# Performance work log

Measured on AMD Instinct MI355X. Metric: run time of the kernel, lower is better.

The kernel has to match this reference:

```python
import jax, jax.numpy as jnp
import numpy as np

EPS = 1e-7  # keras.backend.epsilon()
ROUTING_ITERS = 3

def squash(v, axis=-1):
    s2 = jnp.sum(jnp.square(v), axis=axis, keepdims=True)
    scale = s2 / (1.0 + s2) / jnp.sqrt(s2 + EPS)
    return scale * v

def setup_inputs() -> dict:
    key = jax.random.key(0)
    k1, k2 = jax.random.split(key)
    B, N_IN, D_IN = 128, 648, 16
    N_OUT, D_OUT = 32, 32
    x = jax.random.normal(k1, (B, N_IN, D_IN), dtype=jnp.float32)
    # glorot-uniform-ish scale for W: shape (N_in, num_caps, cap_dim, d_in)
    limit = np.sqrt(6.0 / (D_IN + D_OUT)).astype(np.float32)
    W = jax.random.uniform(k2, (N_IN, N_OUT, D_OUT, D_IN), dtype=jnp.float32,
                           minval=-limit, maxval=limit)
    return {"x": x, "W": W}

def reference(x, W):
    # prediction vectors u_hat: [B, N_in, N_out, D_out]
    # (original tiles inputs then matmuls W @ u; einsum fuses this)
    u_hat = jnp.einsum('njdi,bni->bnjd', W, x)
    B, N_in, N_out, _ = u_hat.shape
    logits = jnp.zeros((B, N_in, N_out, 1), dtype=u_hat.dtype)
    v = None
    for i in range(ROUTING_ITERS):
        c = jax.nn.softmax(logits, axis=2)                      # [B,N_in,N_out,1]
        s = jnp.sum(c * u_hat, axis=1, keepdims=True)           # [B,1,N_out,D_out]
        v = squash(s, axis=-1)                                  # [B,1,N_out,D_out]
        if i < ROUTING_ITERS - 1:
            agreement = jnp.sum(u_hat * v, axis=-1, keepdims=True)
            logits = logits + agreement
    return jnp.squeeze(v, axis=1)                               # [B,N_out,D_out]
```

## Files before the change

### kernel.cpp

```cpp
#include <hip/hip_runtime.h>
#include <hip/hip_fp16.h>
#include <math.h>


#define N_IN 648
#define ELEMS 131072

#define XF_OFF 65536
#define VLD 69632
#define LG 135168
#define ARENA_PH 139264
#define ARENA_P0 132608

typedef __attribute__((ext_vector_type(8))) _Float16 f16x8;
typedef __attribute__((ext_vector_type(16))) float f32x16;

union F16U { uint4 u; f16x8 f; };
union HU { __half h; unsigned short us; };

__device__ __forceinline__ unsigned pkh(float a, float b) {
  HU x, y; x.h = __float2half(a); y.h = __float2half(b);
  return (unsigned)x.us | ((unsigned)y.us << 16);
}
__device__ __forceinline__ float h2f(unsigned short u) {
  HU x; x.us = u; return __half2float(x.h);
}

__device__ __forceinline__ void writeW(char* wbuf, int jS, int d, const float4* r) {
  uint4 h0, h1;
  h0.x = pkh(r[0].x, r[0].y); h0.y = pkh(r[0].z, r[0].w);
  h0.z = pkh(r[1].x, r[1].y); h0.w = pkh(r[1].z, r[1].w);
  h1.x = pkh(r[2].x, r[2].y); h1.y = pkh(r[2].z, r[2].w);
  h1.z = pkh(r[3].x, r[3].y); h1.w = pkh(r[3].z, r[3].w);
  *(uint4*)(wbuf + jS * 1024 + d * 16) = h0;
  *(uint4*)(wbuf + jS * 1024 + 512 + d * 16) = h1;
}
__device__ __forceinline__ void loadW(float4* r, const float* __restrict__ W,
                                      int n, int jS, int d) {
  const float4* rp = (const float4*)(W + (size_t)n * 16384 + jS * 512 + d * 16);
  r[0] = rp[0]; r[1] = rp[1]; r[2] = rp[2]; r[3] = rp[3];
}

__device__ __forceinline__ void store_parts(char* arena, float* __restrict__ parts,
                                            const f32x16* acc, float scale,
                                            int nchunk, int b0, int t) {
  const int w = t >> 6, l = t & 63;
  const int b32 = l & 31, half = l >> 5;
  __syncthreads();
#pragma unroll
  for (int q = 0; q < 4; ++q) {
    const int j = w * 4 + q;
#pragma unroll
    for (int g = 0; g < 4; ++g) {
      float4 v4;
      v4.x = acc[q][g * 4 + 0] * scale;
      v4.y = acc[q][g * 4 + 1] * scale;
      v4.z = acc[q][g * 4 + 2] * scale;
      v4.w = acc[q][g * 4 + 3] * scale;
      *(float4*)(arena + (b32 * 1036 + j * 32 + g * 8 + 4 * half) * 4) = v4;
    }
  }
  __syncthreads();
  float* pb = parts + (size_t)nchunk * ELEMS + (size_t)b0 * 1024;
  const int rb = t >> 4, c16 = t & 15;
#pragma unroll
  for (int q = 0; q < 16; ++q) {
    const int e4 = c16 + q * 16;
    const float4 v4 = *(const float4*)(arena + (rb * 1036 + e4 * 4) * 4);
    *(float4*)(pb + rb * 1024 + e4 * 4) = v4;
  }
}

__device__ __forceinline__ void decode_bid(int bid, int NC, int& nchunk, int& btile) {
  if ((NC & 7) == 0) {
    const int r = bid & 7;
    btile = (bid >> 3) & 3;
    nchunk = (bid >> 5) * 8 + r;
  } else {
    nchunk = bid >> 2;
    btile = bid & 3;
  }
}

__global__ __launch_bounds__(512, 1) void caps_pass0_mfma(
    const float* __restrict__ x, const float* __restrict__ W,
    float* __restrict__ parts, int NC)
{
  __shared__ __align__(16) char arena[ARENA_P0];
  const int t = threadIdx.x;
  const int w = t >> 6, l = t & 63;
  const int jS = t >> 4, m = t & 15;
  int nchunk, btile;
  decode_bid(blockIdx.x, NC, nchunk, btile);
  const int n0 = (N_IN * nchunk) / NC;
  const int n1 = (N_IN * (nchunk + 1)) / NC;
  const int b0 = btile * 32;

  f32x16 acc[4];
#pragma unroll
  for (int q = 0; q < 4; ++q) acc[q] = (f32x16)(0.0f);

  {
    float4 rA[4], rB[4];
    loadW(rA, W, n0, jS, m);
    loadW(rB, W, n0, jS, m + 16);
    writeW(arena, jS, m, rA);
    writeW(arena, jS, m + 16, rB);
    if (t < 64) {
      const float4* xp = (const float4*)(x + ((size_t)(b0 + (t & 31)) * N_IN + n0) * 16 + (t >> 5) * 8);
      *(float4*)(arena + XF_OFF + t * 16) = xp[0];
      *(float4*)(arena + XF_OFF + 1024 + t * 16) = xp[1];
    }
  }

  int cur = 0;
  for (int n = n0; n < n1; ++n) {
    __syncthreads();
    const char* wf = arena + cur * 32768;
    const char* xb = arena + XF_OFF + cur * 2048;
    char* nwf = arena + (cur ^ 1) * 32768;
    char* nxb = arena + XF_OFF + (cur ^ 1) * 2048;
    const bool more = (n + 1 < n1);

    float4 tA[4], tB[4], xt0, xt1;
    if (more) {
      loadW(tA, W, n + 1, jS, m);
      loadW(tB, W, n + 1, jS, m + 16);
      if (t < 64) {
        const float4* xp = (const float4*)(x + ((size_t)(b0 + (t & 31)) * N_IN + n + 1) * 16 + (t >> 5) * 8);
        xt0 = xp[0]; xt1 = xp[1];
      }
    }

    const float4 xw0 = *(const float4*)(xb + l * 16);
    const float4 xw1 = *(const float4*)(xb + 1024 + l * 16);
    F16U bf;
    bf.u = uint4{pkh(xw0.x, xw0.y), pkh(xw0.z, xw0.w),
                 pkh(xw1.x, xw1.y), pkh(xw1.z, xw1.w)};
#pragma unroll
    for (int q = 0; q < 4; ++q) {
      const int j = w * 4 + q;
      const f16x8 af = *(const f16x8*)(wf + j * 1024 + l * 16);
      acc[q] = __builtin_amdgcn_mfma_f32_32x32x16_f16(af, bf.f, acc[q], 0, 0, 0);
    }

    if (more) {
      writeW(nwf, jS, m, tA);
      writeW(nwf, jS, m + 16, tB);
      if (t < 64) {
        *(float4*)(nxb + t * 16) = xt0;
        *(float4*)(nxb + 1024 + t * 16) = xt1;
      }
    }
    cur ^= 1;
  }
  store_parts(arena, parts, acc, 0.03125f, nchunk, b0, t);
}

__global__ __launch_bounds__(512, 1) void caps_phase_mfma(
    const float* __restrict__ x, const float* __restrict__ W,
    const float* __restrict__ v,
    float* __restrict__ parts, int NC)
{
  __shared__ __align__(16) char arena[ARENA_PH];
  const int t = threadIdx.x;
  const int w = t >> 6, l = t & 63;
  const int b32 = l & 31;
  const int jS = t >> 4, m = t & 15;
  int nchunk, btile;
  decode_bid(blockIdx.x, NC, nchunk, btile);
  const int n0 = (N_IN * nchunk) / NC;
  const int n1 = (N_IN * (nchunk + 1)) / NC;
  const int b0 = btile * 32;

#pragma unroll
  for (int r2 = 0; r2 < 2; ++r2) {
    const int j = t >> 4, b = (t & 15) + r2 * 16;
    const float4* gv = (const float4*)(v + (size_t)(b0 + b) * 1024 + j * 32);
    float4 g[8];
#pragma unroll
    for (int q = 0; q < 8; ++q) g[q] = gv[q];
#pragma unroll
    for (int h = 0; h < 2; ++h)
#pragma unroll
      for (int wd = 0; wd < 2; ++wd) {
        const float4 a = g[4 * wd + h];
        const float4 bb = g[4 * wd + h + 2];
        *(uint4*)(arena + VLD + j * 2048 + wd * 1024 + (h * 32 + b) * 16) =
            uint4{pkh(a.x, a.y), pkh(a.z, a.w), pkh(bb.x, bb.y), pkh(bb.z, bb.w)};
      }
  }

  {
    float4 rA[4], rB[4];
    loadW(rA, W, n0, jS, m);
    loadW(rB, W, n0, jS, m + 16);
    writeW(arena, jS, m, rA);
    writeW(arena, jS, m + 16, rB);
    if (t < 64) {
      const float4* xp = (const float4*)(x + ((size_t)(b0 + (t & 31)) * N_IN + n0) * 16 + (t >> 5) * 8);
      *(float4*)(arena + XF_OFF + t * 16) = xp[0];
      *(float4*)(arena + XF_OFF + 1024 + t * 16) = xp[1];
    }
  }

  f32x16 acc[4];
#pragma unroll
  for (int q = 0; q < 4; ++q) acc[q] = (f32x16)(0.0f);

  int cur = 0;
  for (int n = n0; n < n1; ++n) {
    __syncthreads();
    const char* wf = arena + cur * 32768;
    const char* xb = arena + XF_OFF + cur * 2048;
    char* nwf = arena + (cur ^ 1) * 32768;
    char* nxb = arena + XF_OFF + (cur ^ 1) * 2048;
    const bool more = (n + 1 < n1);

    float4 tA[4], xt0, xt1;
    if (more) {
      loadW(tA, W, n + 1, jS, m);
      if (t < 64) {
        const float4* xp = (const float4*)(x + ((size_t)(b0 + (t & 31)) * N_IN + n + 1) * 16 + (t >> 5) * 8);
        xt0 = xp[0]; xt1 = xp[1];
      }
    }

    const float4 xw0 = *(const float4*)(xb + l * 16);
    const float4 xw1 = *(const float4*)(xb + 1024 + l * 16);
    F16U bf;
    bf.u = uint4{pkh(xw0.x, xw0.y), pkh(xw0.z, xw0.w),
                 pkh(xw1.x, xw1.y), pkh(xw1.z, xw1.w)};

#pragma unroll
    for (int q = 0; q < 4; ++q) {
      const int j = w * 4 + q;
      const f16x8 af = *(const f16x8*)(wf + j * 1024 + l * 16);
      f32x16 ut = (f32x16)(0.0f);
      ut = __builtin_amdgcn_mfma_f32_32x32x16_f16(af, bf.f, ut, 0, 0, 0);
      const uint4 va = *(const uint4*)(arena + VLD + j * 2048 + l * 16);
      const uint4 vb = *(const uint4*)(arena + VLD + j * 2048 + 1024 + l * 16);
      const unsigned wd[8] = {va.x, va.y, va.z, va.w, vb.x, vb.y, vb.z, vb.w};
      float a = 0.f;
#pragma unroll
      for (int k = 0; k < 16; ++k) {
        const unsigned short us = (k & 1) ? (unsigned short)(wd[k >> 1] >> 16)
                                          : (unsigned short)(wd[k >> 1] & 0xFFFF);
        a = fmaf(ut[k], h2f(us), a);
      }
      a += __shfl_xor(a, 32);
      if (l < 32)
        *(float*)(arena + LG + (j * 32 + ((b32 ^ j) & 31)) * 4) = a;
    }
    __syncthreads();

    {
      const int jj = t & 31;
#pragma unroll
      for (int r = 0; r < 2; ++r) {
        const int b = r * 16 + (t >> 5);
        float* slot = (float*)(arena + LG + (jj * 32 + ((b ^ jj) & 31)) * 4);
        float lgv = *slot;
        float mx = lgv;
#pragma unroll
        for (int off = 16; off >= 1; off >>= 1) mx = fmaxf(mx, __shfl_xor(mx, off));
        const float e = __expf(lgv - mx);
        float Z = e;
#pragma unroll
        for (int off = 16; off >= 1; off >>= 1) Z += __shfl_xor(Z, off);
        *slot = e / Z;
      }
    }
    if (more) {
      writeW(nwf, jS, m, tA);
      loadW(tA, W, n + 1, jS, m + 16);
      if (t < 64) {
        *(float4*)(nxb + t * 16) = xt0;
        *(float4*)(nxb + 1024 + t * 16) = xt1;
      }
    }
    __syncthreads();

#pragma unroll
    for (int q = 0; q < 4; ++q) {
      const int j = w * 4 + q;
      const float cj = *(const float*)(arena + LG + (j * 32 + ((b32 ^ j) & 31)) * 4);
      F16U yf;
      yf.u = uint4{pkh(cj * xw0.x, cj * xw0.y), pkh(cj * xw0.z, cj * xw0.w),
                   pkh(cj * xw1.x, cj * xw1.y), pkh(cj * xw1.z, cj * xw1.w)};
      const f16x8 af = *(const f16x8*)(wf + j * 1024 + l * 16);
      acc[q] = __builtin_amdgcn_mfma_f32_32x32x16_f16(af, yf.f, acc[q], 0, 0, 0);
    }
    if (more) writeW(nwf, jS, m + 16, tA);
    cur ^= 1;
  }
  store_parts(arena, parts, acc, 1.0f, nchunk, b0, t);
}

__global__ void reduce_squash(const float* __restrict__ parts, int NC,
                              float* __restrict__ out,
                              const float* __restrict__ addprev) {
  const int e = blockIdx.x * 256 + threadIdx.x;
  float s = 0.f;
  for (int c = 0; c < NC; ++c) s += parts[(size_t)c * ELEMS + e];
  float s2 = s * s;
#pragma unroll
  for (int off = 16; off >= 1; off >>= 1) s2 += __shfl_xor(s2, off);
  const float scale = (s2 / (1.0f + s2)) * rsqrtf(s2 + 1e-7f);
  const float val = s * scale;
  out[e] = addprev ? (addprev[e] + val) : val;
}

extern "C" void kernel_launch(void* const* d_in, const int* in_sizes, int n_in,
                              void* d_out, int out_size, void* d_ws, size_t ws_size,
                              hipStream_t stream) {
  const float* x = (const float*)d_in[0];
  const float* W = (const float*)d_in[1];
  float* out = (float*)d_out;

  float* v0 = (float*)d_ws;
  float* vsum = v0 + ELEMS;
  float* parts = vsum + ELEMS;

  int avail = 0;
  if (ws_size / 4 > 2 * (size_t)ELEMS)
    avail = (int)((ws_size / 4 - 2 * (size_t)ELEMS) / ELEMS);
  int NC = avail < 1 ? 1 : (avail > 64 ? 64 : avail);

  const dim3 blk(512);

  caps_pass0_mfma<<<dim3(NC * 4), blk, 0, stream>>>(x, W, parts, NC);
  reduce_squash<<<512, 256, 0, stream>>>(parts, NC, v0, nullptr);

  caps_phase_mfma<<<dim3(NC * 4), blk, 0, stream>>>(x, W, v0, parts, NC);
  reduce_squash<<<512, 256, 0, stream>>>(parts, NC, vsum, v0);

  caps_phase_mfma<<<dim3(NC * 4), blk, 0, stream>>>(x, W, vsum, parts, NC);
  reduce_squash<<<512, 256, 0, stream>>>(parts, NC, out, nullptr);
}
```

Measured before the change: 155.1 us.

## Shrink phase kernel batch tile to 16 and raise occupancy to two blocks

The routing phase kernel now processes 16 batch rows per block instead of 32, so the grid doubles. The kernel keeps v in registers instead of LDS, and shrinks the LDS arena so two blocks can reside per CU. Half the MFMA B-columns are zero-padded, which wastes matrix throughput. W tiles are now loaded twice as often across blocks, and the prefetch of the next W slice moves into the same iteration, reducing overlap. The intent is better latency hiding through occupancy, at the cost of more redundant W traffic and idle MFMA lanes.

```diff
diff --git a/kernel.cpp b/kernel.cpp
--- a/kernel.cpp
+++ b/kernel.cpp
@@ -7,10 +7,11 @@
 #define ELEMS 131072
 
 #define XF_OFF 65536
-#define VLD 69632
-#define LG 135168
-#define ARENA_PH 139264
 #define ARENA_P0 132608
+
+#define PX_OFF 65536
+#define PLG 67584
+#define ARENA_PH 69632
 
 typedef __attribute__((ext_vector_type(8))) _Float16 f16x8;
 typedef __attribute__((ext_vector_type(16))) float f32x16;
@@ -41,9 +42,9 @@
   r[0] = rp[0]; r[1] = rp[1]; r[2] = rp[2]; r[3] = rp[3];
 }
 
-__device__ __forceinline__ void store_parts(char* arena, float* __restrict__ parts,
-                                            const f32x16* acc, float scale,
-                                            int nchunk, int b0, int t) {
+__device__ __forceinline__ void store_parts32(char* arena, float* __restrict__ parts,
+                                              const f32x16* acc, float scale,
+                                              int nchunk, int b0, int t) {
   const int w = t >> 6, l = t & 63;
   const int b32 = l & 31, half = l >> 5;
   __syncthreads();
@@ -68,17 +69,6 @@
     const int e4 = c16 + q * 16;
     const float4 v4 = *(const float4*)(arena + (rb * 1036 + e4 * 4) * 4);
     *(float4*)(pb + rb * 1024 + e4 * 4) = v4;
-  }
-}
-
-__device__ __forceinline__ void decode_bid(int bid, int NC, int& nchunk, int& btile) {
-  if ((NC & 7) == 0) {
-    const int r = bid & 7;
-    btile = (bid >> 3) & 3;
-    nchunk = (bid >> 5) * 8 + r;
-  } else {
-    nchunk = bid >> 2;
-    btile = bid & 3;
   }
 }
 
@@ -91,7 +81,11 @@
   const int w = t >> 6, l = t & 63;
   const int jS = t >> 4, m = t & 15;
   int nchunk, btile;
-  decode_bid(blockIdx.x, NC, nchunk, btile);
+  if ((NC & 7) == 0) {
+    const int r = blockIdx.x & 7;
+    btile = (blockIdx.x >> 3) & 3;
+    nchunk = (blockIdx.x >> 5) * 8 + r;
+  } else { nchunk = blockIdx.x >> 2; btile = blockIdx.x & 3; }
   const int n0 = (N_IN * nchunk) / NC;
   const int n1 = (N_IN * (nchunk + 1)) / NC;
   const int b0 = btile * 32;
@@ -154,10 +148,10 @@
     }
     cur ^= 1;
   }
-  store_parts(arena, parts, acc, 0.03125f, nchunk, b0, t);
-}
-
-__global__ __launch_bounds__(512, 1) void caps_phase_mfma(
+  store_parts32(arena, parts, acc, 0.03125f, nchunk, b0, t);
+}
+
+__global__ __launch_bounds__(512, 2) void caps_phase_mfma(
     const float* __restrict__ x, const float* __restrict__ W,
     const float* __restrict__ v,
     float* __restrict__ parts, int NC)
@@ -165,30 +159,34 @@
   __shared__ __align__(16) char arena[ARENA_PH];
   const int t = threadIdx.x;
   const int w = t >> 6, l = t & 63;
-  const int b32 = l & 31;
+  const int b32 = l & 31, half = l >> 5;
+  const int b16 = b32 & 15;
+  const bool bact = (b32 < 16);
   const int jS = t >> 4, m = t & 15;
+
   int nchunk, btile;
-  decode_bid(blockIdx.x, NC, nchunk, btile);
+  if ((NC & 7) == 0) {
+    const int r = blockIdx.x & 7;
+    btile = (blockIdx.x >> 3) & 7;
+    nchunk = (blockIdx.x >> 6) * 8 + r;
+  } else { nchunk = blockIdx.x >> 3; btile = blockIdx.x & 7; }
   const int n0 = (N_IN * nchunk) / NC;
   const int n1 = (N_IN * (nchunk + 1)) / NC;
-  const int b0 = btile * 32;
-
-#pragma unroll
-  for (int r2 = 0; r2 < 2; ++r2) {
-    const int j = t >> 4, b = (t & 15) + r2 * 16;
-    const float4* gv = (const float4*)(v + (size_t)(b0 + b) * 1024 + j * 32);
-    float4 g[8];
-#pragma unroll
-    for (int q = 0; q < 8; ++q) g[q] = gv[q];
-#pragma unroll
-    for (int h = 0; h < 2; ++h)
-#pragma unroll
-      for (int wd = 0; wd < 2; ++wd) {
-        const float4 a = g[4 * wd + h];
-        const float4 bb = g[4 * wd + h + 2];
-        *(uint4*)(arena + VLD + j * 2048 + wd * 1024 + (h * 32 + b) * 16) =
-            uint4{pkh(a.x, a.y), pkh(a.z, a.w), pkh(bb.x, bb.y), pkh(bb.z, bb.w)};
-      }
+  const int b0 = btile * 16;
+
+  unsigned vw[4][8];
+  {
+    const int bv = b0 + b16;
+#pragma unroll
+    for (int q = 0; q < 4; ++q) {
+      const int j = w * 4 + q;
+#pragma unroll
+      for (int g = 0; g < 4; ++g) {
+        const float4 g4 = *(const float4*)(v + (size_t)bv * 1024 + j * 32 + g * 8 + 4 * half);
+        vw[q][2 * g]     = pkh(g4.x, g4.y);
+        vw[q][2 * g + 1] = pkh(g4.z, g4.w);
+      }
+    }
   }
 
   {
@@ -198,9 +196,9 @@
     writeW(arena, jS, m, rA);
     writeW(arena, jS, m + 16, rB);
     if (t < 64) {
-      const float4* xp = (const float4*)(x + ((size_t)(b0 + (t & 31)) * N_IN + n0) * 16 + (t >> 5) * 8);
-      *(float4*)(arena + XF_OFF + t * 16) = xp[0];
-      *(float4*)(arena + XF_OFF + 1024 + t * 16) = xp[1];
+      const int c = t & 1, b = (t >> 1) & 15, h = t >> 5;
+      *(float4*)(arena + PX_OFF + t * 16) =
+          *(const float4*)(x + ((size_t)(b0 + b) * N_IN + n0) * 16 + h * 8 + c * 4);
     }
   }
 
@@ -212,22 +210,16 @@
   for (int n = n0; n < n1; ++n) {
     __syncthreads();
     const char* wf = arena + cur * 32768;
-    const char* xb = arena + XF_OFF + cur * 2048;
+    const char* xb = arena + PX_OFF + cur * 1024;
     char* nwf = arena + (cur ^ 1) * 32768;
-    char* nxb = arena + XF_OFF + (cur ^ 1) * 2048;
+    char* nxb = arena + PX_OFF + (cur ^ 1) * 1024;
     const bool more = (n + 1 < n1);
 
-    float4 tA[4], xt0, xt1;
-    if (more) {
-      loadW(tA, W, n + 1, jS, m);
-      if (t < 64) {
-        const float4* xp = (const float4*)(x + ((size_t)(b0 + (t & 31)) * N_IN + n + 1) * 16 + (t >> 5) * 8);
-        xt0 = xp[0]; xt1 = xp[1];
-      }
-    }
-
-    const float4 xw0 = *(const float4*)(xb + l * 16);
-    const float4 xw1 = *(const float4*)(xb + 1024 + l * 16);
+    float4 xw0 = float4{0.f, 0.f, 0.f, 0.f}, xw1 = xw0;
+    if (bact) {
+      xw0 = *(const float4*)(xb + (half * 32 + b16 * 2 + 0) * 16);
+      xw1 = *(const float4*)(xb + (half * 32 + b16 * 2 + 1) * 16);
+    }
     F16U bf;
     bf.u = uint4{pkh(xw0.x, xw0.y), pkh(xw0.z, xw0.w),
                  pkh(xw1.x, xw1.y), pkh(xw1.z, xw1.w)};
@@ -238,45 +230,43 @@
       const f16x8 af = *(const f16x8*)(wf + j * 1024 + l * 16);
       f32x16 ut = (f32x16)(0.0f);
       ut = __builtin_amdgcn_mfma_f32_32x32x16_f16(af, bf.f, ut, 0, 0, 0);
-      const uint4 va = *(const uint4*)(arena + VLD + j * 2048 + l * 16);
-      const uint4 vb = *(const uint4*)(arena + VLD + j * 2048 + 1024 + l * 16);
-      const unsigned wd[8] = {va.x, va.y, va.z, va.w, vb.x, vb.y, vb.z, vb.w};
       float a = 0.f;
 #pragma unroll
       for (int k = 0; k < 16; ++k) {
-        const unsigned short us = (k & 1) ? (unsigned short)(wd[k >> 1] >> 16)
-                                          : (unsigned short)(wd[k >> 1] & 0xFFFF);
+        const unsigned short us = (k & 1) ? (unsigned short)(vw[q][k >> 1] >> 16)
+                                          : (unsigned short)(vw[q][k >> 1] & 0xFFFF);
         a = fmaf(ut[k], h2f(us), a);
       }
       a += __shfl_xor(a, 32);
-      if (l < 32)
-        *(float*)(arena + LG + (j * 32 + ((b32 ^ j) & 31)) * 4) = a;
+      if (l < 16)
+        *(float*)(arena + PLG + (j * 16 + ((l + j) & 15)) * 4) = a;
     }
     __syncthreads();
 
     {
-      const int jj = t & 31;
-#pragma unroll
-      for (int r = 0; r < 2; ++r) {
-        const int b = r * 16 + (t >> 5);
-        float* slot = (float*)(arena + LG + (jj * 32 + ((b ^ jj) & 31)) * 4);
-        float lgv = *slot;
-        float mx = lgv;
-#pragma unroll
-        for (int off = 16; off >= 1; off >>= 1) mx = fmaxf(mx, __shfl_xor(mx, off));
-        const float e = __expf(lgv - mx);
-        float Z = e;
-#pragma unroll
-        for (int off = 16; off >= 1; off >>= 1) Z += __shfl_xor(Z, off);
-        *slot = e / Z;
-      }
-    }
+      const int jj = t & 31, b = t >> 5;
+      float* slot = (float*)(arena + PLG + (jj * 16 + ((b + jj) & 15)) * 4);
+      float lgv = *slot;
+      float mx = lgv;
+#pragma unroll
+      for (int off = 16; off >= 1; off >>= 1) mx = fmaxf(mx, __shfl_xor(mx, off));
+      const float e = __expf(lgv - mx);
+      float Z = e;
+#pragma unroll
+      for (int off = 16; off >= 1; off >>= 1) Z += __shfl_xor(Z, off);
+      *slot = e / Z;
+    }
+
     if (more) {
-      writeW(nwf, jS, m, tA);
-      loadW(tA, W, n + 1, jS, m + 16);
+      float4 rA[4], rB[4];
+      loadW(rA, W, n + 1, jS, m);
+      loadW(rB, W, n + 1, jS, m + 16);
+      writeW(nwf, jS, m, rA);
+      writeW(nwf, jS, m + 16, rB);
       if (t < 64) {
-        *(float4*)(nxb + t * 16) = xt0;
-        *(float4*)(nxb + 1024 + t * 16) = xt1;
+        const int c = t & 1, b = (t >> 1) & 15, h = t >> 5;
+        *(float4*)(nxb + t * 16) =
+            *(const float4*)(x + ((size_t)(b0 + b) * N_IN + n + 1) * 16 + h * 8 + c * 4);
       }
     }
     __syncthreads();
@@ -284,17 +274,43 @@
 #pragma unroll
     for (int q = 0; q < 4; ++q) {
       const int j = w * 4 + q;
-      const float cj = *(const float*)(arena + LG + (j * 32 + ((b32 ^ j) & 31)) * 4);
+      const float cj = *(const float*)(arena + PLG + (j * 16 + ((b16 + j) & 15)) * 4);
       F16U yf;
       yf.u = uint4{pkh(cj * xw0.x, cj * xw0.y), pkh(cj * xw0.z, cj * xw0.w),
                    pkh(cj * xw1.x, cj * xw1.y), pkh(cj * xw1.z, cj * xw1.w)};
       const f16x8 af = *(const f16x8*)(wf + j * 1024 + l * 16);
       acc[q] = __builtin_amdgcn_mfma_f32_32x32x16_f16(af, yf.f, acc[q], 0, 0, 0);
     }
-    if (more) writeW(nwf, jS, m + 16, tA);
     cur ^= 1;
   }
-  store_parts(arena, parts, acc, 1.0f, nchunk, b0, t);
+
+  __syncthreads();
+#pragma unroll
+  for (int q = 0; q < 4; ++q) {
+    const int j = w * 4 + q;
+    if (bact) {
+#pragma unroll
+      for (int g = 0; g < 4; ++g) {
+        float4 v4;
+        v4.x = acc[q][g * 4 + 0];
+        v4.y = acc[q][g * 4 + 1];
+        v4.z = acc[q][g * 4 + 2];
+        v4.w = acc[q][g * 4 + 3];
+        *(float4*)(arena + (b16 * 1036 + j * 32 + g * 8 + 4 * half) * 4) = v4;
+      }
+    }
+  }
+  __syncthreads();
+  {
+    float* pb = parts + (size_t)nchunk * ELEMS + (size_t)b0 * 1024;
+    const int rb = t >> 5, c32 = t & 31;
+#pragma unroll
+    for (int q = 0; q < 8; ++q) {
+      const int e4 = c32 + q * 32;
+      const float4 v4 = *(const float4*)(arena + (rb * 1036 + e4 * 4) * 4);
+      *(float4*)(pb + rb * 1024 + e4 * 4) = v4;
+    }
+  }
 }
 
 __global__ void reduce_squash(const float* __restrict__ parts, int NC,
@@ -332,9 +348,9 @@
   caps_pass0_mfma<<<dim3(NC * 4), blk, 0, stream>>>(x, W, parts, NC);
   reduce_squash<<<512, 256, 0, stream>>>(parts, NC, v0, nullptr);
 
-  caps_phase_mfma<<<dim3(NC * 4), blk, 0, stream>>>(x, W, v0, parts, NC);
+  caps_phase_mfma<<<dim3(NC * 8), blk, 0, stream>>>(x, W, v0, parts, NC);
   reduce_squash<<<512, 256, 0, stream>>>(parts, NC, vsum, v0);
 
-  caps_phase_mfma<<<dim3(NC * 4), blk, 0, stream>>>(x, W, vsum, parts, NC);
+  caps_phase_mfma<<<dim3(NC * 8), blk, 0, stream>>>(x, W, vsum, parts, NC);
   reduce_squash<<<512, 256, 0, stream>>>(parts, NC, out, nullptr);
 }
```

Measured after the change: 225.9 us. 45.7% more time.

## Pre-convert W to fp16 once, store partial sums in fp16, keep v in registers

Applied to the files above, without the earlier changes.

Adds a prologue kernel that converts W to a pre-swizzled fp16 layout in the workspace, so the three routing kernels load half the bytes and copy straight into LDS without per-iteration conversion. Partial sums written per chunk are now stored as fp16, halving the traffic of the store and of the reduction. The v operand in the phase kernel now lives in registers instead of LDS, which shrinks the LDS arena. In exchange there is an extra launch and a W-sized write and read, fp16 partials lose precision when NC chunks are accumulated, and the kernel needs a larger workspace at fixed offsets.

```diff
diff --git a/kernel.cpp b/kernel.cpp
--- a/kernel.cpp
+++ b/kernel.cpp
@@ -6,11 +6,12 @@
 #define N_IN 648
 #define ELEMS 131072
 
+#define WF16_OFF 1048576
+#define PARTS_OFF 22282240
+
 #define XF_OFF 65536
-#define VLD 69632
-#define LG 135168
-#define ARENA_PH 139264
-#define ARENA_P0 132608
+#define LG 69632
+#define ARENA 132608
 
 typedef __attribute__((ext_vector_type(8))) _Float16 f16x8;
 typedef __attribute__((ext_vector_type(16))) float f32x16;
@@ -41,7 +42,31 @@
   r[0] = rp[0]; r[1] = rp[1]; r[2] = rp[2]; r[3] = rp[3];
 }
 
-__device__ __forceinline__ void store_parts(char* arena, float* __restrict__ parts,
+__global__ __launch_bounds__(512) void cvt_w_f16(const float* __restrict__ W,
+                                                 char* __restrict__ wf) {
+  const int n = blockIdx.x;
+  const int t = threadIdx.x;
+  const int jS = t >> 4, m = t & 15;
+  float4 rA[4], rB[4];
+  loadW(rA, W, n, jS, m);
+  loadW(rB, W, n, jS, m + 16);
+  char* dst = wf + (size_t)n * 32768;
+  writeW(dst, jS, m, rA);
+  writeW(dst, jS, m + 16, rB);
+}
+
+__device__ __forceinline__ void copyW(char* dst, const char* __restrict__ src, int t) {
+  uint4 c0 = *(const uint4*)(src + 0 * 8192 + t * 16);
+  uint4 c1 = *(const uint4*)(src + 1 * 8192 + t * 16);
+  uint4 c2 = *(const uint4*)(src + 2 * 8192 + t * 16);
+  uint4 c3 = *(const uint4*)(src + 3 * 8192 + t * 16);
+  *(uint4*)(dst + 0 * 8192 + t * 16) = c0;
+  *(uint4*)(dst + 1 * 8192 + t * 16) = c1;
+  *(uint4*)(dst + 2 * 8192 + t * 16) = c2;
+  *(uint4*)(dst + 3 * 8192 + t * 16) = c3;
+}
+
+__device__ __forceinline__ void store_parts(char* arena, __half* __restrict__ parts,
                                             const f32x16* acc, float scale,
                                             int nchunk, int b0, int t) {
   const int w = t >> 6, l = t & 63;
@@ -61,13 +86,15 @@
     }
   }
   __syncthreads();
-  float* pb = parts + (size_t)nchunk * ELEMS + (size_t)b0 * 1024;
+  char* pb = (char*)(parts + (size_t)nchunk * ELEMS + (size_t)b0 * 1024);
   const int rb = t >> 4, c16 = t & 15;
 #pragma unroll
-  for (int q = 0; q < 16; ++q) {
-    const int e4 = c16 + q * 16;
-    const float4 v4 = *(const float4*)(arena + (rb * 1036 + e4 * 4) * 4);
-    *(float4*)(pb + rb * 1024 + e4 * 4) = v4;
+  for (int q = 0; q < 8; ++q) {
+    const int g8 = c16 + q * 16;
+    const float4 a = *(const float4*)(arena + (rb * 1036 + g8 * 8) * 4);
+    const float4 b = *(const float4*)(arena + (rb * 1036 + g8 * 8 + 4) * 4);
+    *(uint4*)(pb + rb * 2048 + g8 * 16) =
+        uint4{pkh(a.x, a.y), pkh(a.z, a.w), pkh(b.x, b.y), pkh(b.z, b.w)};
   }
 }
 
@@ -83,13 +110,12 @@
 }
 
 __global__ __launch_bounds__(512, 1) void caps_pass0_mfma(
-    const float* __restrict__ x, const float* __restrict__ W,
-    float* __restrict__ parts, int NC)
+    const float* __restrict__ x, const char* __restrict__ wf16,
+    __half* __restrict__ parts, int NC)
 {
-  __shared__ __align__(16) char arena[ARENA_P0];
+  __shared__ __align__(16) char arena[ARENA];
   const int t = threadIdx.x;
   const int w = t >> 6, l = t & 63;
-  const int jS = t >> 4, m = t & 15;
   int nchunk, btile;
   decode_bid(blockIdx.x, NC, nchunk, btile);
   const int n0 = (N_IN * nchunk) / NC;
@@ -100,17 +126,11 @@
 #pragma unroll
   for (int q = 0; q < 4; ++q) acc[q] = (f32x16)(0.0f);
 
-  {
-    float4 rA[4], rB[4];
-    loadW(rA, W, n0, jS, m);
-    loadW(rB, W, n0, jS, m + 16);
-    writeW(arena, jS, m, rA);
-    writeW(arena, jS, m + 16, rB);
-    if (t < 64) {
-      const float4* xp = (const float4*)(x + ((size_t)(b0 + (t & 31)) * N_IN + n0) * 16 + (t >> 5) * 8);
-      *(float4*)(arena + XF_OFF + t * 16) = xp[0];
-      *(float4*)(arena + XF_OFF + 1024 + t * 16) = xp[1];
-    }
+  copyW(arena, wf16 + (size_t)n0 * 32768, t);
+  if (t < 64) {
+    const float4* xp = (const float4*)(x + ((size_t)(b0 + (t & 31)) * N_IN + n0) * 16 + (t >> 5) * 8);
+    *(float4*)(arena + XF_OFF + t * 16) = xp[0];
+    *(float4*)(arena + XF_OFF + 1024 + t * 16) = xp[1];
   }
 
   int cur = 0;
@@ -122,16 +142,6 @@
     char* nxb = arena + XF_OFF + (cur ^ 1) * 2048;
     const bool more = (n + 1 < n1);
 
-    float4 tA[4], tB[4], xt0, xt1;
-    if (more) {
-      loadW(tA, W, n + 1, jS, m);
-      loadW(tB, W, n + 1, jS, m + 16);
-      if (t < 64) {
-        const float4* xp = (const float4*)(x + ((size_t)(b0 + (t & 31)) * N_IN + n + 1) * 16 + (t >> 5) * 8);
-        xt0 = xp[0]; xt1 = xp[1];
-      }
-    }
-
     const float4 xw0 = *(const float4*)(xb + l * 16);
     const float4 xw1 = *(const float4*)(xb + 1024 + l * 16);
     F16U bf;
@@ -145,11 +155,11 @@
     }
 
     if (more) {
-      writeW(nwf, jS, m, tA);
-      writeW(nwf, jS, m + 16, tB);
+      copyW(nwf, wf16 + (size_t)(n + 1) * 32768, t);
       if (t < 64) {
-        *(float4*)(nxb + t * 16) = xt0;
-        *(float4*)(nxb + 1024 + t * 16) = xt1;
+        const float4* xp = (const float4*)(x + ((size_t)(b0 + (t & 31)) * N_IN + n + 1) * 16 + (t >> 5) * 8);
+        *(float4*)(nxb + t * 16) = xp[0];
+        *(float4*)(nxb + 1024 + t * 16) = xp[1];
       }
     }
     cur ^= 1;
@@ -158,50 +168,40 @@
 }
 
 __global__ __launch_bounds__(512, 1) void caps_phase_mfma(
-    const float* __restrict__ x, const float* __restrict__ W,
+    const float* __restrict__ x, const char* __restrict__ wf16,
     const float* __restrict__ v,
-    float* __restrict__ parts, int NC)
+    __half* __restrict__ parts, int NC)
 {
-  __shared__ __align__(16) char arena[ARENA_PH];
+  __shared__ __align__(16) char arena[ARENA];
   const int t = threadIdx.x;
   const int w = t >> 6, l = t & 63;
-  const int b32 = l & 31;
-  const int jS = t >> 4, m = t & 15;
+  const int b32 = l & 31, half = l >> 5;
   int nchunk, btile;
   decode_bid(blockIdx.x, NC, nchunk, btile);
   const int n0 = (N_IN * nchunk) / NC;
   const int n1 = (N_IN * (nchunk + 1)) / NC;
   const int b0 = btile * 32;
 
-#pragma unroll
-  for (int r2 = 0; r2 < 2; ++r2) {
-    const int j = t >> 4, b = (t & 15) + r2 * 16;
-    const float4* gv = (const float4*)(v + (size_t)(b0 + b) * 1024 + j * 32);
-    float4 g[8];
-#pragma unroll
-    for (int q = 0; q < 8; ++q) g[q] = gv[q];
-#pragma unroll
-    for (int h = 0; h < 2; ++h)
-#pragma unroll
-      for (int wd = 0; wd < 2; ++wd) {
-        const float4 a = g[4 * wd + h];
-        const float4 bb = g[4 * wd + h + 2];
-        *(uint4*)(arena + VLD + j * 2048 + wd * 1024 + (h * 32 + b) * 16) =
-            uint4{pkh(a.x, a.y), pkh(a.z, a.w), pkh(bb.x, bb.y), pkh(bb.z, bb.w)};
-      }
-  }
-
+  unsigned vw[4][8];
   {
-    float4 rA[4], rB[4];
-    loadW(rA, W, n0, jS, m);
-    loadW(rB, W, n0, jS, m + 16);
-    writeW(arena, jS, m, rA);
-    writeW(arena, jS, m + 16, rB);
-    if (t < 64) {
-      const float4* xp = (const float4*)(x + ((size_t)(b0 + (t & 31)) * N_IN + n0) * 16 + (t >> 5) * 8);
-      *(float4*)(arena + XF_OFF + t * 16) = xp[0];
-      *(float4*)(arena + XF_OFF + 1024 + t * 16) = xp[1];
-    }
+    const int bv = b0 + b32;
+#pragma unroll
+    for (int q = 0; q < 4; ++q) {
+      const int j = w * 4 + q;
+#pragma unroll
+      for (int g = 0; g < 4; ++g) {
+        const float4 g4 = *(const float4*)(v + (size_t)bv * 1024 + j * 32 + g * 8 + 4 * half);
+        vw[q][2 * g]     = pkh(g4.x, g4.y);
+        vw[q][2 * g + 1] = pkh(g4.z, g4.w);
+      }
+    }
+  }
+
+  copyW(arena, wf16 + (size_t)n0 * 32768, t);
+  if (t < 64) {
+    const float4* xp = (const float4*)(x + ((size_t)(b0 + (t & 31)) * N_IN + n0) * 16 + (t >> 5) * 8);
+    *(float4*)(arena + XF_OFF + t * 16) = xp[0];
+    *(float4*)(arena + XF_OFF + 1024 + t * 16) = xp[1];
   }
 
   f32x16 acc[4];
@@ -217,15 +217,6 @@
     char* nxb = arena + XF_OFF + (cur ^ 1) * 2048;
     const bool more = (n + 1 < n1);
 
-    float4 tA[4], xt0, xt1;
-    if (more) {
-      loadW(tA, W, n + 1, jS, m);
-      if (t < 64) {
-        const float4* xp = (const float4*)(x + ((size_t)(b0 + (t & 31)) * N_IN + n + 1) * 16 + (t >> 5) * 8);
-        xt0 = xp[0]; xt1 = xp[1];
-      }
-    }
-
     const float4 xw0 = *(const float4*)(xb + l * 16);
     const float4 xw1 = *(const float4*)(xb + 1024 + l * 16);
     F16U bf;
@@ -238,14 +229,11 @@
       const f16x8 af = *(const f16x8*)(wf + j * 1024 + l * 16);
       f32x16 ut = (f32x16)(0.0f);
       ut = __builtin_amdgcn_mfma_f32_32x32x16_f16(af, bf.f, ut, 0, 0, 0);
-      const uint4 va = *(const uint4*)(arena + VLD + j * 2048 + l * 16);
-      const uint4 vb = *(const uint4*)(arena + VLD + j * 2048 + 1024 + l * 16);
-      const unsigned wd[8] = {va.x, va.y, va.z, va.w, vb.x, vb.y, vb.z, vb.w};
       float a = 0.f;
 #pragma unroll
       for (int k = 0; k < 16; ++k) {
-        const unsigned short us = (k & 1) ? (unsigned short)(wd[k >> 1] >> 16)
-                                          : (unsigned short)(wd[k >> 1] & 0xFFFF);
+        const unsigned short us = (k & 1) ? (unsigned short)(vw[q][k >> 1] >> 16)
+                                          : (unsigned short)(vw[q][k >> 1] & 0xFFFF);
         a = fmaf(ut[k], h2f(us), a);
       }
       a += __shfl_xor(a, 32);
@@ -271,12 +259,13 @@
         *slot = e / Z;
       }
     }
+
     if (more) {
-      writeW(nwf, jS, m, tA);
-      loadW(tA, W, n + 1, jS, m + 16);
+      copyW(nwf, wf16 + (size_t)(n + 1) * 32768, t);
       if (t < 64) {
-        *(float4*)(nxb + t * 16) = xt0;
-        *(float4*)(nxb + 1024 + t * 16) = xt1;
+        const float4* xp = (const float4*)(x + ((size_t)(b0 + (t & 31)) * N_IN + n + 1) * 16 + (t >> 5) * 8);
+        *(float4*)(nxb + t * 16) = xp[0];
+        *(float4*)(nxb + 1024 + t * 16) = xp[1];
       }
     }
     __syncthreads();
@@ -291,18 +280,17 @@
       const f16x8 af = *(const f16x8*)(wf + j * 1024 + l * 16);
       acc[q] = __builtin_amdgcn_mfma_f32_32x32x16_f16(af, yf.f, acc[q], 0, 0, 0);
     }
-    if (more) writeW(nwf, jS, m + 16, tA);
     cur ^= 1;
   }
   store_parts(arena, parts, acc, 1.0f, nchunk, b0, t);
 }
 
-__global__ void reduce_squash(const float* __restrict__ parts, int NC,
+__global__ void reduce_squash(const unsigned short* __restrict__ parts, int NC,
                               float* __restrict__ out,
                               const float* __restrict__ addprev) {
   const int e = blockIdx.x * 256 + threadIdx.x;
   float s = 0.f;
-  for (int c = 0; c < NC; ++c) s += parts[(size_t)c * ELEMS + e];
+  for (int c = 0; c < NC; ++c) s += h2f(parts[(size_t)c * ELEMS + e]);
   float s2 = s * s;
 #pragma unroll
   for (int off = 16; off >= 1; off >>= 1) s2 += __shfl_xor(s2, off);
@@ -320,21 +308,23 @@
 
   float* v0 = (float*)d_ws;
   float* vsum = v0 + ELEMS;
-  float* parts = vsum + ELEMS;
-
-  int avail = 0;
-  if (ws_size / 4 > 2 * (size_t)ELEMS)
-    avail = (int)((ws_size / 4 - 2 * (size_t)ELEMS) / ELEMS);
-  int NC = avail < 1 ? 1 : (avail > 64 ? 64 : avail);
+  char* wf16 = (char*)d_ws + WF16_OFF;
+  __half* parts = (__half*)((char*)d_ws + PARTS_OFF);
+
+  size_t rem = ws_size > (size_t)PARTS_OFF ? ws_size - PARTS_OFF : 0;
+  int NC = (int)(rem / (ELEMS * 2));
+  NC = NC < 1 ? 1 : (NC > 64 ? 64 : NC);
 
   const dim3 blk(512);
 
-  caps_pass0_mfma<<<dim3(NC * 4), blk, 0, stream>>>(x, W, parts, NC);
-  reduce_squash<<<512, 256, 0, stream>>>(parts, NC, v0, nullptr);
-
-  caps_phase_mfma<<<dim3(NC * 4), blk, 0, stream>>>(x, W, v0, parts, NC);
-  reduce_squash<<<512, 256, 0, stream>>>(parts, NC, vsum, v0);
-
-  caps_phase_mfma<<<dim3(NC * 4), blk, 0, stream>>>(x, W, vsum, parts, NC);
-  reduce_squash<<<512, 256, 0, stream>>>(parts, NC, out, nullptr);
-}
+  cvt_w_f16<<<dim3(N_IN), blk, 0, stream>>>(W, wf16);
+
+  caps_pass0_mfma<<<dim3(NC * 4), blk, 0, stream>>>(x, wf16, parts, NC);
+  reduce_squash<<<512, 256, 0, stream>>>((const unsigned short*)parts, NC, v0, nullptr);
+
+  caps_phase_mfma<<<dim3(NC * 4), blk, 0, stream>>>(x, wf16, v0, parts, NC);
+  reduce_squash<<<512, 256, 0, stream>>>((const unsigned short*)parts, NC, vsum, v0);
+
+  caps_phase_mfma<<<dim3(NC * 4), blk, 0, stream>>>(x, wf16, vsum, parts, NC);
+  reduce_squash<<<512, 256, 0, stream>>>((const unsigned short*)parts, NC, out, nullptr);
+}
```

Result: no change. 152.8 us (-1.5%).
